# Kernel optimization log

Hardware: AMD Instinct MI355X
Metric: run time of the kernel (lower is better)

## Reference

```python
import jax, jax.numpy as jnp
import numpy as np
from jax import lax

EPS = 1e-5

def gelu(x):
    return jax.nn.gelu(x, approximate=False)  # torch nn.GELU default (erf)

def conv1d(x, w, b):
    # x: (N, Cin, L), w: (Cout, Cin, K), SAME padding, stride 1
    y = lax.conv_general_dilated(x, w, window_strides=(1,), padding='SAME',
                                 dimension_numbers=('NCH', 'OIH', 'NCH'))
    return y + b[None, :, None]

def setup_inputs() -> dict:
    key = jax.random.key(0)
    ks = jax.random.split(key, 16)
    B, C, P, L, D = 8, 129, 62, 20, 256
    s = lambda k, shape, fan: jax.random.normal(k, shape, jnp.float32) * (1.0 / np.sqrt(fan))
    return {
        'x': jax.random.normal(ks[0], (B, C, P, L), jnp.float32),
        'conv1_w': s(ks[1], (64, 1, 3), 3),   'conv1_b': jnp.zeros((64,), jnp.float32),
        'conv2_w': s(ks[2], (128, 64, 3), 192), 'conv2_b': jnp.zeros((128,), jnp.float32),
        'conv3_w': s(ks[3], (D, 128, 3), 384),  'conv3_b': jnp.zeros((D,), jnp.float32),
        'mix_w': s(ks[4], (C, C), C), 'mix_b': jnp.zeros((C,), jnp.float32),
        'ln_w': jnp.ones((C,), jnp.float32), 'ln_b': jnp.zeros((C,), jnp.float32),
        'proj_w': s(ks[5], (D, D), D), 'proj_b': jnp.zeros((D,), jnp.float32),
    }

def reference(x, conv1_w, conv1_b, conv2_w, conv2_b, conv3_w, conv3_b,
              mix_w, mix_b, ln_w, ln_b, proj_w, proj_b):
    B, C, P, L = x.shape
    D = conv3_w.shape[0]
    # temporal conv stack over flattened (B*C*P, 1, L)
    h = x.reshape(B * C * P, 1, L)
    h = gelu(conv1d(h, conv1_w, conv1_b))
    h = gelu(conv1d(h, conv2_w, conv2_b))
    N, Ch, Lh = h.shape
    h = h.reshape(N, Ch, Lh // 2, 2).max(axis=-1)  # MaxPool1d(2)
    h = gelu(conv1d(h, conv3_w, conv3_b))
    feat = h.mean(axis=-1)                                  # (B*C*P, D)
    feat = feat.reshape(B, C, P, D).transpose(0, 2, 1, 3)   # (B, P, C, D)
    t = feat.reshape(B * P, C, D).transpose(0, 2, 1)        # (B*P, D, C) == per-feature slices
    # channel_mix: Linear(C,C) + GELU + LayerNorm(C), vectorized over the dim axis
    m = gelu(jnp.einsum('ndc,oc->ndo', t, mix_w) + mix_b)
    mu = m.mean(axis=-1, keepdims=True)
    var = ((m - mu) ** 2).mean(axis=-1, keepdims=True)
    m = (m - mu) * lax.rsqrt(var + EPS) * ln_w + ln_b
    mixed = m.transpose(0, 2, 1).reshape(B, P, C, D)
    out = jnp.einsum('bpcd,ed->bpce', mixed, proj_w) + proj_b
    return out.transpose(0, 2, 1, 3)                        # (B, C, P, D)
```

## Files before the change

### kernel.cpp

```cpp
#include <hip/hip_runtime.h>

#define B_ 8
#define C_ 129
#define P_ 62
#define L_ 20
#define D_ 256
#define NSEG (B_*C_*P_)
#define N2   (B_*P_)
#define SEGB 8
#define NWG  (NSEG/SEGB)

#define S1 1416
#define S2 1544

#define FT_STRIDE 168
#define MT_STRIDE 264

typedef short short8 __attribute__((ext_vector_type(8)));
typedef float f32x4  __attribute__((ext_vector_type(4)));

__device__ __forceinline__ float gelu_f(float x) {
    float u  = 0.70710678f * x;
    float au = __builtin_fabsf(u);
    float t  = __builtin_amdgcn_rcpf(fmaf(0.3275911f, au, 1.0f));
    float p  = fmaf(1.061405429f, t, -1.453152027f);
    p = fmaf(p, t, 1.421413741f);
    p = fmaf(p, t, -0.284496736f);
    p = fmaf(p, t, 0.254829592f);
    p = p * t;
    float e  = __builtin_amdgcn_exp2f(-1.4426950409f * au * au);
    float ea = fmaf(-p, e, 1.0f);
    float er = copysignf(ea, u);
    return 0.5f * x * (1.0f + er);
}
__device__ __forceinline__ unsigned short f2bf(float f) {
    unsigned u = __float_as_uint(f);
    u = u + 0x7FFFu + ((u >> 16) & 1u);
    return (unsigned short)(u >> 16);
}

__global__ void prep_kernel(const float* __restrict__ w2, const float* __restrict__ w3,
                            const float* __restrict__ mw, const float* __restrict__ pw,
                            const float* __restrict__ mixb, const float* __restrict__ lnw,
                            const float* __restrict__ lnb,
                            unsigned short* __restrict__ A2p, unsigned short* __restrict__ A3p,
                            unsigned short* __restrict__ mixA, unsigned short* __restrict__ projA,
                            float* __restrict__ bmixp, float* __restrict__ lnwp,
                            float* __restrict__ lnbp) {
    int idx = blockIdx.x * blockDim.x + threadIdx.x;
    int stride = gridDim.x * blockDim.x;
    for (int f = idx; f < 6*8*64*8; f += stride) {
        int j = f & 7, ln = (f >> 3) & 63, mt = (f >> 9) & 7, kt = f >> 12;
        int co = mt*16 + (ln & 15);
        int k  = kt >> 1;
        int ci = (kt & 1)*32 + (ln >> 4)*8 + j;
        A2p[f] = f2bf(w2[(co*64 + ci)*3 + k]);
    }
    for (int f = idx; f < 12*16*64*8; f += stride) {
        int j = f & 7, ln = (f >> 3) & 63, mt = (f >> 9) & 15, kt = f >> 13;
        int co = mt*16 + (ln & 15);
        int k  = kt >> 2;
        int ci = (kt & 3)*32 + (ln >> 4)*8 + j;
        A3p[f] = f2bf(w3[(co*128 + ci)*3 + k]);
    }
    for (int f = idx; f < 5*9*64*8; f += stride) {
        int j = f & 7, ln = (f >> 3) & 63;
        int mt = (f >> 9) % 9, kt = (f >> 9) / 9;
        int o = mt*16 + (ln & 15);
        int c = kt*32 + (ln >> 4)*8 + j;
        mixA[f] = (o < 129 && c < 129) ? f2bf(mw[o*129 + c]) : (unsigned short)0;
    }
    for (int f = idx; f < 8*16*64*8; f += stride) {
        int j = f & 7, ln = (f >> 3) & 63, mt = (f >> 9) & 15, kt = f >> 13;
        int e = mt*16 + (ln & 15);
        int d = kt*32 + (ln >> 4)*8 + j;
        projA[f] = f2bf(pw[e*256 + d]);
    }
    for (int i = idx; i < 144; i += stride) {
        bmixp[i] = (i < 129) ? mixb[i] : 0.f;
        lnwp[i]  = (i < 129) ? lnw[i]  : 0.f;
        lnbp[i]  = (i < 129) ? lnb[i]  : 0.f;
    }
}

__global__ __launch_bounds__(512, 4) void conv_mfma_kernel(
    const float* __restrict__ x,
    const float* __restrict__ w1, const float* __restrict__ b1,
    const unsigned short* __restrict__ A2p, const float* __restrict__ b2,
    const unsigned short* __restrict__ A3p, const float* __restrict__ b3,
    float* __restrict__ feat)
{
    __shared__ __align__(16) unsigned short h1T[SEGB * S1];
    __shared__ __align__(16) unsigned short hpT[SEGB * S2];
    __shared__ float xs[SEGB][22];

    const int t = threadIdx.x;
    const int wave = t >> 6, lane = t & 63;
    const int sL = lane & 15, gL = lane >> 4;
    const int seg8 = sL & 7, hi8 = sL >> 3;
    const int seg0 = blockIdx.x * SEGB;

    for (int idx = t; idx < SEGB*22; idx += 512) {
        int s = idx / 22, i = idx % 22;
        float v = 0.f;
        if (i >= 1 && i <= 20) v = x[(seg0 + s)*L_ + i - 1];
        xs[s][i] = v;
    }
    for (int idx = t; idx < SEGB*64; idx += 512) {
        int s = idx >> 6, ci = idx & 63;
        h1T[s*S1 + ci] = 0;
        h1T[s*S1 + 21*64 + ci] = 0;
    }
    for (int idx = t; idx < SEGB*128; idx += 512) {
        int s = idx >> 7, co = idx & 127;
        hpT[s*S2 + co] = 0;
        hpT[s*S2 + 11*128 + co] = 0;
    }
    __syncthreads();

    {
        int seg = wave;
        int cp = (lane >> 1) & 31, ph = lane & 1;
        int ci0 = cp * 2;
        float wa0 = w1[ci0*3+0], wa1 = w1[ci0*3+1], wa2 = w1[ci0*3+2], ba = b1[ci0];
        float wb0 = w1[ci0*3+3], wb1 = w1[ci0*3+4], wb2 = w1[ci0*3+5], bb = b1[ci0+1];
        unsigned short* dst = &h1T[seg*S1 + ci0];
        #pragma unroll
        for (int i = 0; i < 10; ++i) {
            int l = ph*10 + i;
            float x0 = xs[seg][l], x1 = xs[seg][l+1], x2v = xs[seg][l+2];
            float va = fmaf(x0, wa0, fmaf(x1, wa1, fmaf(x2v, wa2, ba)));
            float vb = fmaf(x0, wb0, fmaf(x1, wb1, fmaf(x2v, wb2, bb)));
            unsigned pk = (unsigned)f2bf(gelu_f(va)) | ((unsigned)f2bf(gelu_f(vb)) << 16);
            *(unsigned*)(dst + (l+1)*64) = pk;
        }
    }
    __syncthreads();

    {
        const int mh = wave & 3, ng = wave >> 2;
        f32x4 acc[2][5];
        #pragma unroll
        for (int mi = 0; mi < 2; ++mi)
            #pragma unroll
            for (int n = 0; n < 5; ++n) acc[mi][n] = (f32x4){0.f,0.f,0.f,0.f};

        const unsigned short* h1base = &h1T[seg8*S1 + (ng*10 + hi8)*64 + gL*8];
        #pragma unroll
        for (int h = 0; h < 2; ++h) {
            short8 br[11];
            #pragma unroll
            for (int r = 0; r < 11; ++r)
                br[r] = *(const short8*)(h1base + r*64 + h*32);
            #pragma unroll
            for (int k = 0; k < 3; ++k) {
                int kt = k*2 + h;
                short8 a0 = *(const short8*)(A2p + (((kt*8 + mh*2 + 0)*64 + lane) << 3));
                short8 a1 = *(const short8*)(A2p + (((kt*8 + mh*2 + 1)*64 + lane) << 3));
                #pragma unroll
                for (int n = 0; n < 5; ++n) {
                    acc[0][n] = __builtin_amdgcn_mfma_f32_16x16x32_bf16(a0, br[2*n+k], acc[0][n], 0, 0, 0);
                    acc[1][n] = __builtin_amdgcn_mfma_f32_16x16x32_bf16(a1, br[2*n+k], acc[1][n], 0, 0, 0);
                }
            }
        }
        #pragma unroll
        for (int mi = 0; mi < 2; ++mi) {
            int mt = mh*2 + mi;
            int co0 = mt*16 + gL*4;
            float4 bb = *(const float4*)(b2 + co0);
            float bbr[4] = {bb.x, bb.y, bb.z, bb.w};
            #pragma unroll
            for (int n = 0; n < 5; ++n) {
                int lp = ng*5 + n;
                float pv[4];
                #pragma unroll
                for (int r = 0; r < 4; ++r) {
                    float g = gelu_f(acc[mi][n][r] + bbr[r]);
                    pv[r] = fmaxf(g, __shfl_xor(g, 8));
                }
                if (hi8 == 0) {
                    unsigned short pk[4];
                    #pragma unroll
                    for (int r = 0; r < 4; ++r) pk[r] = f2bf(pv[r]);
                    *(uint2*)&hpT[seg8*S2 + (lp+1)*128 + co0] = *(uint2*)pk;
                }
            }
        }
    }
    __syncthreads();

    {
        f32x4 acc[2][5];
        #pragma unroll
        for (int mi = 0; mi < 2; ++mi)
            #pragma unroll
            for (int n = 0; n < 5; ++n) acc[mi][n] = (f32x4){0.f,0.f,0.f,0.f};

        const unsigned short* hpbase = &hpT[seg8*S2 + hi8*128 + gL*8];
        #pragma unroll
        for (int q = 0; q < 4; ++q) {
            short8 br[11];
            #pragma unroll
            for (int r = 0; r < 11; ++r)
                br[r] = *(const short8*)(hpbase + r*128 + q*32);
            #pragma unroll
            for (int k = 0; k < 3; ++k) {
                int kt = k*4 + q;
                short8 a0 = *(const short8*)(A3p + (((kt*16 + wave*2 + 0)*64 + lane) << 3));
                short8 a1 = *(const short8*)(A3p + (((kt*16 + wave*2 + 1)*64 + lane) << 3));
                #pragma unroll
                for (int n = 0; n < 5; ++n) {
                    acc[0][n] = __builtin_amdgcn_mfma_f32_16x16x32_bf16(a0, br[2*n+k], acc[0][n], 0, 0, 0);
                    acc[1][n] = __builtin_amdgcn_mfma_f32_16x16x32_bf16(a1, br[2*n+k], acc[1][n], 0, 0, 0);
                }
            }
        }
        int seg = seg0 + seg8;
        int bI = seg / (C_*P_);
        int rem = seg % (C_*P_);
        int c = rem / P_, p = rem % P_;
        float* frow = feat + (((size_t)(bI*P_ + p)*C_ + c) << 8);
        #pragma unroll
        for (int mi = 0; mi < 2; ++mi) {
            int co0 = (wave*2 + mi)*16 + gL*4;
            float4 bv = *(const float4*)(b3 + co0);
            float bbr[4] = {bv.x, bv.y, bv.z, bv.w};
            float sum[4] = {0.f, 0.f, 0.f, 0.f};
            #pragma unroll
            for (int n = 0; n < 5; ++n)
                #pragma unroll
                for (int r = 0; r < 4; ++r)
                    sum[r] += gelu_f(acc[mi][n][r] + bbr[r]);
            #pragma unroll
            for (int r = 0; r < 4; ++r)
                sum[r] += __shfl_xor(sum[r], 8);
            if (hi8 == 0) {
                float4 o;
                o.x = sum[0]*0.1f; o.y = sum[1]*0.1f; o.z = sum[2]*0.1f; o.w = sum[3]*0.1f;
                *(float4*)(frow + co0) = o;
            }
        }
    }
}

__global__ __launch_bounds__(512, 2) void mix_proj_kernel(
    const float* __restrict__ feat,
    const unsigned short* __restrict__ mixA, const float* __restrict__ bmixp,
    const float* __restrict__ lnwp, const float* __restrict__ lnbp,
    const unsigned short* __restrict__ projA, const float* __restrict__ proj_b,
    float* __restrict__ out)
{
    __shared__ __align__(16) unsigned short ulds[256*FT_STRIDE];
    unsigned short* fT = ulds;
    unsigned short* mT = ulds;

    const int t = threadIdx.x;
    const int wave = t >> 6, lane = t & 63;
    const int sL = lane & 15, gL = lane >> 4;
    const int n2 = blockIdx.x;
    const int b = n2 / P_, p = n2 % P_;

    const float* fbase = feat + (size_t)n2 * C_ * 256;
    for (int idx = t; idx < 129*256; idx += 512) {
        int c = idx >> 8, d = idx & 255;
        fT[d*FT_STRIDE + c] = f2bf(fbase[idx]);
    }
    for (int idx = t; idx < 256*31; idx += 512) {
        int d = idx / 31, c = 129 + idx % 31;
        fT[d*FT_STRIDE + c] = 0;
    }
    __syncthreads();

    f32x4 acc[9][2];
    #pragma unroll
    for (int mt = 0; mt < 9; ++mt)
        #pragma unroll
        for (int nt = 0; nt < 2; ++nt) acc[mt][nt] = (f32x4){0.f,0.f,0.f,0.f};

    #pragma unroll
    for (int kt = 0; kt < 5; ++kt) {
        short8 bb[2];
        #pragma unroll
        for (int nt = 0; nt < 2; ++nt) {
            int d = (wave*2 + nt)*16 + sL;
            bb[nt] = *(const short8*)&fT[d*FT_STRIDE + kt*32 + gL*8];
        }
        #pragma unroll
        for (int mt = 0; mt < 9; ++mt) {
            short8 a = *(const short8*)(mixA + (((kt*9 + mt)*64 + lane) << 3));
            #pragma unroll
            for (int nt = 0; nt < 2; ++nt)
                acc[mt][nt] = __builtin_amdgcn_mfma_f32_16x16x32_bf16(a, bb[nt], acc[mt][nt], 0, 0, 0);
        }
    }

    float sum[2] = {0.f, 0.f}, sq[2] = {0.f, 0.f};
    #pragma unroll
    for (int mt = 0; mt < 9; ++mt) {
        float4 bv = *(const float4*)(bmixp + mt*16 + gL*4);
        float bbr[4] = {bv.x, bv.y, bv.z, bv.w};
        #pragma unroll
        for (int nt = 0; nt < 2; ++nt) {
            #pragma unroll
            for (int r = 0; r < 4; ++r) {
                int o = mt*16 + gL*4 + r;
                float g = (o < 129) ? gelu_f(acc[mt][nt][r] + bbr[r]) : 0.f;
                acc[mt][nt][r] = g;
                sum[nt] += g;
                sq[nt]  += g*g;
            }
        }
    }
    float mu[2], rs[2];
    #pragma unroll
    for (int nt = 0; nt < 2; ++nt) {
        float s = sum[nt], q = sq[nt];
        s += __shfl_xor(s, 16); q += __shfl_xor(q, 16);
        s += __shfl_xor(s, 32); q += __shfl_xor(q, 32);
        mu[nt] = s * (1.f/129.f);
        float var = q * (1.f/129.f) - mu[nt]*mu[nt];
        rs[nt] = rsqrtf(var + 1e-5f);
    }

    __syncthreads();

    #pragma unroll
    for (int mt = 0; mt < 9; ++mt) {
        float4 lw = *(const float4*)(lnwp + mt*16 + gL*4);
        float4 lb = *(const float4*)(lnbp + mt*16 + gL*4);
        float lwr[4] = {lw.x, lw.y, lw.z, lw.w};
        float lbr[4] = {lb.x, lb.y, lb.z, lb.w};
        #pragma unroll
        for (int nt = 0; nt < 2; ++nt) {
            int d = (wave*2 + nt)*16 + sL;
            #pragma unroll
            for (int r = 0; r < 4; ++r) {
                int o = mt*16 + gL*4 + r;
                float y = (acc[mt][nt][r] - mu[nt]) * rs[nt] * lwr[r] + lbr[r];
                mT[o*MT_STRIDE + d] = f2bf(y);
            }
        }
    }
    __syncthreads();

    f32x4 pacc[2][9];
    #pragma unroll
    for (int mi = 0; mi < 2; ++mi)
        #pragma unroll
        for (int nt = 0; nt < 9; ++nt) pacc[mi][nt] = (f32x4){0.f,0.f,0.f,0.f};

    #pragma unroll
    for (int kt = 0; kt < 8; ++kt) {
        short8 a[2];
        #pragma unroll
        for (int mi = 0; mi < 2; ++mi)
            a[mi] = *(const short8*)(projA + (((kt*16 + wave*2 + mi)*64 + lane) << 3));
        #pragma unroll
        for (int nt = 0; nt < 9; ++nt) {
            short8 bb = *(const short8*)&mT[(nt*16 + sL)*MT_STRIDE + kt*32 + gL*8];
            #pragma unroll
            for (int mi = 0; mi < 2; ++mi)
                pacc[mi][nt] = __builtin_amdgcn_mfma_f32_16x16x32_bf16(a[mi], bb, pacc[mi][nt], 0, 0, 0);
        }
    }

    #pragma unroll
    for (int mi = 0; mi < 2; ++mi) {
        int e0 = (wave*2 + mi)*16 + gL*4;
        float4 pb4 = *(const float4*)(proj_b + e0);
        #pragma unroll
        for (int nt = 0; nt < 9; ++nt) {
            int c = nt*16 + sL;
            if (c < 129) {
                float4 o4;
                o4.x = pacc[mi][nt][0] + pb4.x;
                o4.y = pacc[mi][nt][1] + pb4.y;
                o4.z = pacc[mi][nt][2] + pb4.z;
                o4.w = pacc[mi][nt][3] + pb4.w;
                *(float4*)&out[(((size_t)(b*C_ + c)*P_) + p)*256 + e0] = o4;
            }
        }
    }
}

extern "C" void kernel_launch(void* const* d_in, const int* in_sizes, int n_in,
                              void* d_out, int out_size, void* d_ws, size_t ws_size,
                              hipStream_t stream) {
    (void)in_sizes; (void)n_in; (void)out_size; (void)ws_size;
    const float* x    = (const float*)d_in[0];
    const float* w1   = (const float*)d_in[1];
    const float* b1   = (const float*)d_in[2];
    const float* w2   = (const float*)d_in[3];
    const float* b2   = (const float*)d_in[4];
    const float* w3   = (const float*)d_in[5];
    const float* b3   = (const float*)d_in[6];
    const float* mixw = (const float*)d_in[7];
    const float* mixb = (const float*)d_in[8];
    const float* lnw  = (const float*)d_in[9];
    const float* lnb  = (const float*)d_in[10];
    const float* pw   = (const float*)d_in[11];
    const float* pb   = (const float*)d_in[12];
    float* out = (float*)d_out;
    float* ws  = (float*)d_ws;

    float* feat = ws;
    unsigned short* A2p  = (unsigned short*)(ws + 16379904);
    unsigned short* A3p  = A2p + 24576;
    unsigned short* mixA = A3p + 98304;
    unsigned short* projA = mixA + 23040;
    float* bmixp = (float*)(projA + 65536);
    float* lnwp  = bmixp + 144;
    float* lnbp  = lnwp + 144;

    prep_kernel<<<256, 256, 0, stream>>>(w2, w3, mixw, pw, mixb, lnw, lnb,
                                         A2p, A3p, mixA, projA, bmixp, lnwp, lnbp);
    conv_mfma_kernel<<<NWG, 512, 0, stream>>>(x, w1, b1, A2p, b2, A3p, b3, feat);
    mix_proj_kernel<<<N2, 512, 0, stream>>>(feat, mixA, bmixp, lnwp, lnbp, projA, pb, out);
}
```

Before: 388.5 us.

## Use cheaper GELU approximation, hardware bf16 pack, and bf16 intermediate features

Replaces the 5-term erf polynomial in GELU with a shorter 3-term approximation, uses the v_cvt_pk_bf16_f32 instruction instead of manual rounding, and stores the intermediate feature tensor as bf16 instead of fp32. The mix kernel then reads packed bf16 pairs. This cuts ALU work in the GELU-heavy conv kernel and halves the global traffic for the features. In exchange, the lower-order erf approximation adds error to every GELU.

```diff
diff --git a/kernel.cpp b/kernel.cpp
--- a/kernel.cpp
+++ b/kernel.cpp
@@ -20,23 +20,29 @@
 typedef float f32x4  __attribute__((ext_vector_type(4)));
 
 __device__ __forceinline__ float gelu_f(float x) {
-    float u  = 0.70710678f * x;
-    float au = __builtin_fabsf(u);
-    float t  = __builtin_amdgcn_rcpf(fmaf(0.3275911f, au, 1.0f));
-    float p  = fmaf(1.061405429f, t, -1.453152027f);
-    p = fmaf(p, t, 1.421413741f);
-    p = fmaf(p, t, -0.284496736f);
-    p = fmaf(p, t, 0.254829592f);
-    p = p * t;
-    float e  = __builtin_amdgcn_exp2f(-1.4426950409f * au * au);
-    float ea = fmaf(-p, e, 1.0f);
-    float er = copysignf(ea, u);
-    return 0.5f * x * (1.0f + er);
+    float u   = 0.70710678f * x;
+    float au  = __builtin_fabsf(u);
+    float den = fmaf(0.47047f, au, 1.0f);
+    float t   = __builtin_amdgcn_rcpf(den);
+    float q   = fmaf(0.7478556f, t, -0.0958798f);
+    q = fmaf(q, t, 0.3480242f);
+    float P  = q * t;
+    float z  = (-1.4426950409f * au) * au;
+    float e  = __builtin_amdgcn_exp2f(z);
+    float ea = fmaf(-P, e, 1.0f);
+    float er = copysignf(ea, x);
+    float hx = 0.5f * x;
+    return fmaf(hx, er, hx);
 }
 __device__ __forceinline__ unsigned short f2bf(float f) {
     unsigned u = __float_as_uint(f);
     u = u + 0x7FFFu + ((u >> 16) & 1u);
     return (unsigned short)(u >> 16);
+}
+__device__ __forceinline__ unsigned cvt_pk_bf16(float lo, float hi) {
+    unsigned r;
+    asm("v_cvt_pk_bf16_f32 %0, %1, %2" : "=v"(r) : "v"(lo), "v"(hi));
+    return r;
 }
 
 __global__ void prep_kernel(const float* __restrict__ w2, const float* __restrict__ w3,
@@ -88,7 +94,7 @@
     const float* __restrict__ w1, const float* __restrict__ b1,
     const unsigned short* __restrict__ A2p, const float* __restrict__ b2,
     const unsigned short* __restrict__ A3p, const float* __restrict__ b3,
-    float* __restrict__ feat)
+    unsigned short* __restrict__ feat)
 {
     __shared__ __align__(16) unsigned short h1T[SEGB * S1];
     __shared__ __align__(16) unsigned short hpT[SEGB * S2];
@@ -131,8 +137,7 @@
             float x0 = xs[seg][l], x1 = xs[seg][l+1], x2v = xs[seg][l+2];
             float va = fmaf(x0, wa0, fmaf(x1, wa1, fmaf(x2v, wa2, ba)));
             float vb = fmaf(x0, wb0, fmaf(x1, wb1, fmaf(x2v, wb2, bb)));
-            unsigned pk = (unsigned)f2bf(gelu_f(va)) | ((unsigned)f2bf(gelu_f(vb)) << 16);
-            *(unsigned*)(dst + (l+1)*64) = pk;
+            *(unsigned*)(dst + (l+1)*64) = cvt_pk_bf16(gelu_f(va), gelu_f(vb));
         }
     }
     __syncthreads();
@@ -180,10 +185,10 @@
                     pv[r] = fmaxf(g, __shfl_xor(g, 8));
                 }
                 if (hi8 == 0) {
-                    unsigned short pk[4];
-                    #pragma unroll
-                    for (int r = 0; r < 4; ++r) pk[r] = f2bf(pv[r]);
-                    *(uint2*)&hpT[seg8*S2 + (lp+1)*128 + co0] = *(uint2*)pk;
+                    uint2 pk;
+                    pk.x = cvt_pk_bf16(pv[0], pv[1]);
+                    pk.y = cvt_pk_bf16(pv[2], pv[3]);
+                    *(uint2*)&hpT[seg8*S2 + (lp+1)*128 + co0] = pk;
                 }
             }
         }
@@ -220,7 +225,7 @@
         int bI = seg / (C_*P_);
         int rem = seg % (C_*P_);
         int c = rem / P_, p = rem % P_;
-        float* frow = feat + (((size_t)(bI*P_ + p)*C_ + c) << 8);
+        unsigned short* frow = feat + (((size_t)(bI*P_ + p)*C_ + c) << 8);
         #pragma unroll
         for (int mi = 0; mi < 2; ++mi) {
             int co0 = (wave*2 + mi)*16 + gL*4;
@@ -236,16 +241,17 @@
             for (int r = 0; r < 4; ++r)
                 sum[r] += __shfl_xor(sum[r], 8);
             if (hi8 == 0) {
-                float4 o;
-                o.x = sum[0]*0.1f; o.y = sum[1]*0.1f; o.z = sum[2]*0.1f; o.w = sum[3]*0.1f;
-                *(float4*)(frow + co0) = o;
+                uint2 o;
+                o.x = cvt_pk_bf16(sum[0]*0.1f, sum[1]*0.1f);
+                o.y = cvt_pk_bf16(sum[2]*0.1f, sum[3]*0.1f);
+                *(uint2*)(frow + co0) = o;
             }
         }
     }
 }
 
 __global__ __launch_bounds__(512, 2) void mix_proj_kernel(
-    const float* __restrict__ feat,
+    const unsigned short* __restrict__ feat,
     const unsigned short* __restrict__ mixA, const float* __restrict__ bmixp,
     const float* __restrict__ lnwp, const float* __restrict__ lnbp,
     const unsigned short* __restrict__ projA, const float* __restrict__ proj_b,
@@ -261,10 +267,13 @@
     const int n2 = blockIdx.x;
     const int b = n2 / P_, p = n2 % P_;
 
-    const float* fbase = feat + (size_t)n2 * C_ * 256;
-    for (int idx = t; idx < 129*256; idx += 512) {
-        int c = idx >> 8, d = idx & 255;
-        fT[d*FT_STRIDE + c] = f2bf(fbase[idx]);
+    const unsigned* fbase32 = (const unsigned*)(feat + (size_t)n2 * C_ * 256);
+    for (int idx = t; idx < 129*128; idx += 512) {
+        int c = idx >> 7, q = idx & 127;
+        unsigned v = fbase32[idx];
+        int d0 = q * 2;
+        fT[d0*FT_STRIDE + c]     = (unsigned short)(v & 0xFFFFu);
+        fT[(d0+1)*FT_STRIDE + c] = (unsigned short)(v >> 16);
     }
     for (int idx = t; idx < 256*31; idx += 512) {
         int d = idx / 31, c = 129 + idx % 31;
@@ -404,7 +413,7 @@
     float* out = (float*)d_out;
     float* ws  = (float*)d_ws;
 
-    float* feat = ws;
+    unsigned short* feat = (unsigned short*)ws;
     unsigned short* A2p  = (unsigned short*)(ws + 16379904);
     unsigned short* A3p  = A2p + 24576;
     unsigned short* mixA = A3p + 98304;
```

New measurement: 360.5 us. 7.2% less time.
